# Kernel tuning notes

Measured on AMD Instinct MI355X. Metric: run time of the kernel, lower is better.

The kernel has to match this reference:

```python
import jax, jax.numpy as jnp
import numpy as np

N_NODES = 20000
N_EDGES = 160000
F_IN = 512
HIDDEN = 512
N_CLASSES = 40


def setup_inputs() -> dict:
    key = jax.random.key(0)
    k1, k2, k3, k4 = jax.random.split(key, 4)
    x = jax.random.normal(k1, (N_NODES, F_IN), dtype=jnp.float32)
    edge_index = jax.random.randint(k2, (2, N_EDGES), 0, N_NODES, dtype=jnp.int64)
    # Glorot-ish init scale for the linear weights
    W1 = jax.random.normal(k3, (F_IN, HIDDEN), dtype=jnp.float32) / np.sqrt(F_IN)
    b1 = jnp.zeros((HIDDEN,), dtype=jnp.float32)
    W2 = jax.random.normal(k4, (HIDDEN, N_CLASSES), dtype=jnp.float32) / np.sqrt(HIDDEN)
    b2 = jnp.zeros((N_CLASSES,), dtype=jnp.float32)
    return {"x": x, "edge_index": edge_index, "W1": W1, "b1": b1, "W2": W2, "b2": b2}


def _gcn_conv(x, W, b, src, dst, n_nodes):
    """PyG GCNConv: h = D^-1/2 (A+I) D^-1/2 (x W) + b, self-loops already in src/dst."""
    h = x @ W  # [N, out]
    deg = jax.ops.segment_sum(jnp.ones_like(dst, dtype=h.dtype), dst, num_segments=n_nodes)
    deg_inv_sqrt = jnp.where(deg > 0, jax.lax.rsqrt(jnp.maximum(deg, 1.0)), 0.0)
    norm = deg_inv_sqrt[src] * deg_inv_sqrt[dst]  # [E]
    msg = h[src] * norm[:, None]  # [E, out]
    return jax.ops.segment_sum(msg, dst, num_segments=n_nodes) + b


def reference(x, edge_index, W1, b1, W2, b2):
    n = x.shape[0]
    loop = jnp.arange(n, dtype=edge_index.dtype)
    src = jnp.concatenate([edge_index[0], loop])  # add self-loops
    dst = jnp.concatenate([edge_index[1], loop])
    h = _gcn_conv(x, W1, b1, src, dst, n)
    h = jax.nn.relu(h)
    # dropout(p=0.5) is identity in eval mode
    out = _gcn_conv(h, W2, b2, src, dst, n)
    return out
```

## Files before the change

kernel.cpp:

```cpp
#include <hip/hip_runtime.h>
#include <hip/hip_bf16.h>
#include <stdint.h>

#define N_NODES  20000
#define N_EDGES  160000
#define N_CLS    40
#define M_PAD    20096
#define CNT_PAD  20480
#define CAP      64

typedef __bf16 bf16;
typedef __attribute__((ext_vector_type(8))) __bf16 bf16x8;
typedef __attribute__((ext_vector_type(4))) float floatx4;

__device__ inline floatx4 zero4() { floatx4 z = {0.f, 0.f, 0.f, 0.f}; return z; }

typedef __attribute__((address_space(3))) uint32_t lds_u32;
typedef __attribute__((address_space(1))) const uint32_t glb_u32;
__device__ inline void ldst16(const bf16* g, bf16* l) {
    __builtin_amdgcn_global_load_lds((glb_u32*)g, (lds_u32*)l, 16, 0, 0);
}

struct Params {
    const float* x; const int* ei; const float* W1; const float* b1;
    const float* W2; const float* b2; float* out;
    bf16 *xb, *w1t, *w2p, *h1; float* h2;
    int *cnt, *colb;
};

#define S0_ZERO 20
#define S0_CONV 5024
#define S0_W1T  128
#define S0_W2P  96
#define S0_TOT  (S0_ZERO + S0_CONV + S0_W1T + S0_W2P)
#define NB_G1   640
#define NB_FILL 625

__global__ __launch_bounds__(256) void k_s0(Params p) {
    const int vb = blockIdx.x, tid = threadIdx.x;
    if (vb < S0_ZERO) {
        int4* dz = (int4*)(p.cnt) + vb * 256 + tid;
        *dz = make_int4(0, 0, 0, 0);
    } else if (vb < S0_ZERO + S0_CONV) {
        long e0 = ((long)(vb - S0_ZERO) * 256 + tid) * 8;
        int row = (int)(e0 >> 9);
        bf16x8 v;
        if (row < N_NODES) {
            const float4* ptr = (const float4*)(p.x + e0);
            float4 f0 = ptr[0], f1 = ptr[1];
            v[0] = (bf16)f0.x; v[1] = (bf16)f0.y; v[2] = (bf16)f0.z; v[3] = (bf16)f0.w;
            v[4] = (bf16)f1.x; v[5] = (bf16)f1.y; v[6] = (bf16)f1.z; v[7] = (bf16)f1.w;
        } else {
            for (int j = 0; j < 8; ++j) v[j] = (bf16)0.f;
        }
        *(bf16x8*)(p.xb + e0) = v;
    } else if (vb < S0_ZERO + S0_CONV + S0_W1T) {
        int t  = (vb - S0_ZERO - S0_CONV) * 256 + tid;
        int n  = t & 511;
        int k0 = (t >> 9) * 8;
        bf16x8 v;
        for (int j = 0; j < 8; ++j) v[j] = (bf16)p.W1[((k0 + j) << 9) + n];
        *(bf16x8*)(p.w1t + n * 512 + k0) = v;
    } else {
        int t = (vb - S0_ZERO - S0_CONV - S0_W1T) * 256 + tid;
        int j = t & 7; int e = t >> 3;
        int lane = e & 63; e >>= 6;
        int nb = e % 3; int kt = e / 3;
        int k = kt * 32 + (lane >> 4) * 8 + j;
        int n = nb * 16 + (lane & 15);
        float v = (n < N_CLS) ? p.W2[k * N_CLS + n] : 0.f;
        p.w2p[t] = (bf16)v;
    }
}

__global__ __launch_bounds__(256) void k_g1f(Params p) {
    if (blockIdx.x >= NB_G1) {
        int e = (blockIdx.x - NB_G1) * 256 + threadIdx.x;
        if (e < N_EDGES) {
            int d = p.ei[N_EDGES + e];
            int j = atomicAdd(&p.cnt[d], 1);
            if (j < CAP) p.colb[d * CAP + j] = p.ei[e];
        }
        return;
    }
    const int g  = blockIdx.x;
    const int mi = (g >> 5) * 8 + (g & 7);
    const int ni = (g >> 3) & 3;
    if (mi >= 157) return;
    __shared__ bf16 As[2][128 * 32];
    __shared__ bf16 Bs[2][128 * 32];
    const int tid  = threadIdx.x;
    const int lane = tid & 63;
    const int w    = tid >> 6;
    const int wm   = w >> 1, wn = w & 1;
    const int m0   = mi * 128;
    const int n0   = ni * 128;
    const int fr   = lane & 15, fq = lane >> 4;

    floatx4 acc[4][4];
    for (int mb = 0; mb < 4; ++mb)
        for (int nb = 0; nb < 4; ++nb) acc[mb][nb] = zero4();

    const int sr = lane >> 2;
    const int sk = (lane & 3) * 8;
    const bf16* Ag = p.xb  + (long)(m0 + w * 32 + sr) * 512 + sk;
    const bf16* Bg = p.w1t + (long)(n0 + w * 32 + sr) * 512 + sk;
    const int wof = w * 1024;

    ldst16(Ag,            As[0] + wof);
    ldst16(Ag + 16 * 512, As[0] + wof + 512);
    ldst16(Bg,            Bs[0] + wof);
    ldst16(Bg + 16 * 512, Bs[0] + wof + 512);

    for (int kt = 0; kt < 16; ++kt) {
        const int cur = kt & 1, nxt = cur ^ 1;
        __syncthreads();
        if (kt < 15) {
            const int k1 = (kt + 1) * 32;
            ldst16(Ag + k1,            As[nxt] + wof);
            ldst16(Ag + k1 + 16 * 512, As[nxt] + wof + 512);
            ldst16(Bg + k1,            Bs[nxt] + wof);
            ldst16(Bg + k1 + 16 * 512, Bs[nxt] + wof + 512);
        }
        bf16x8 af[4], bfv[4];
        for (int mb = 0; mb < 4; ++mb)
            af[mb]  = *(const bf16x8*)(As[cur] + (wm * 64 + mb * 16 + fr) * 32 + fq * 8);
        for (int nb = 0; nb < 4; ++nb)
            bfv[nb] = *(const bf16x8*)(Bs[cur] + (wn * 64 + nb * 16 + fr) * 32 + fq * 8);
        for (int mb = 0; mb < 4; ++mb)
            for (int nb = 0; nb < 4; ++nb)
                acc[mb][nb] = __builtin_amdgcn_mfma_f32_16x16x32_bf16(af[mb], bfv[nb], acc[mb][nb], 0, 0, 0);
    }
    for (int mb = 0; mb < 4; ++mb)
        for (int nb = 0; nb < 4; ++nb) {
            int row0 = m0 + wm * 64 + mb * 16 + fq * 4;
            int c    = n0 + wn * 64 + nb * 16 + fr;
            for (int r = 0; r < 4; ++r)
                p.h1[(long)(row0 + r) * 512 + c] = (bf16)acc[mb][nb][r];
        }
}

__global__ __launch_bounds__(256) void k_agg1g2(Params p) {
    __shared__ bf16 t[16 * 512];
    const int tid = threadIdx.x, l = tid & 63, w = tid >> 6;
    const int ib = blockIdx.x * 16;

    const float4* bp = (const float4*)(p.b1 + l * 8);
    float4 c0 = bp[0], c1 = bp[1];
    float bb[8] = {c0.x, c0.y, c0.z, c0.w, c1.x, c1.y, c1.z, c1.w};

    for (int q4 = 0; q4 < 4; ++q4) {
        const int r = w * 4 + q4;
        const int i = ib + r;
        bf16x8 o;
        if (i >= N_NODES) {
            for (int j = 0; j < 8; ++j) o[j] = (bf16)0.f;
        } else {
            const int ci = p.cnt[i];
            const float di = rsqrtf((float)(ci + 1));
            float acc[8];
            {
                bf16x8 v = *(const bf16x8*)(p.h1 + (long)i * 512 + l * 8);
                const float wi = di * di;
                for (int j = 0; j < 8; ++j) acc[j] = (float)v[j] * wi;
            }
            const int e1 = ci < CAP ? ci : CAP;
            const int* rowcol = p.colb + (long)i * CAP;
            int e = 0;
            for (; e + 8 <= e1; e += 8) {
                int4 sa = *(const int4*)(rowcol + e);
                int4 sb = *(const int4*)(rowcol + e + 4);
                float wgt[8];
                wgt[0] = rsqrtf((float)(p.cnt[sa.x] + 1)) * di;
                wgt[1] = rsqrtf((float)(p.cnt[sa.y] + 1)) * di;
                wgt[2] = rsqrtf((float)(p.cnt[sa.z] + 1)) * di;
                wgt[3] = rsqrtf((float)(p.cnt[sa.w] + 1)) * di;
                wgt[4] = rsqrtf((float)(p.cnt[sb.x] + 1)) * di;
                wgt[5] = rsqrtf((float)(p.cnt[sb.y] + 1)) * di;
                wgt[6] = rsqrtf((float)(p.cnt[sb.z] + 1)) * di;
                wgt[7] = rsqrtf((float)(p.cnt[sb.w] + 1)) * di;
                bf16x8 u[8];
                u[0] = *(const bf16x8*)(p.h1 + (long)sa.x * 512 + l * 8);
                u[1] = *(const bf16x8*)(p.h1 + (long)sa.y * 512 + l * 8);
                u[2] = *(const bf16x8*)(p.h1 + (long)sa.z * 512 + l * 8);
                u[3] = *(const bf16x8*)(p.h1 + (long)sa.w * 512 + l * 8);
                u[4] = *(const bf16x8*)(p.h1 + (long)sb.x * 512 + l * 8);
                u[5] = *(const bf16x8*)(p.h1 + (long)sb.y * 512 + l * 8);
                u[6] = *(const bf16x8*)(p.h1 + (long)sb.z * 512 + l * 8);
                u[7] = *(const bf16x8*)(p.h1 + (long)sb.w * 512 + l * 8);
                for (int q = 0; q < 8; ++q)
                    for (int j = 0; j < 8; ++j) acc[j] += (float)u[q][j] * wgt[q];
            }
            for (; e + 4 <= e1; e += 4) {
                int4 ss = *(const int4*)(rowcol + e);
                float w0 = rsqrtf((float)(p.cnt[ss.x] + 1)) * di;
                float w1 = rsqrtf((float)(p.cnt[ss.y] + 1)) * di;
                float w2 = rsqrtf((float)(p.cnt[ss.z] + 1)) * di;
                float w3 = rsqrtf((float)(p.cnt[ss.w] + 1)) * di;
                bf16x8 u0 = *(const bf16x8*)(p.h1 + (long)ss.x * 512 + l * 8);
                bf16x8 u1 = *(const bf16x8*)(p.h1 + (long)ss.y * 512 + l * 8);
                bf16x8 u2 = *(const bf16x8*)(p.h1 + (long)ss.z * 512 + l * 8);
                bf16x8 u3 = *(const bf16x8*)(p.h1 + (long)ss.w * 512 + l * 8);
                for (int j = 0; j < 8; ++j)
                    acc[j] += (float)u0[j] * w0 + (float)u1[j] * w1 + (float)u2[j] * w2 + (float)u3[j] * w3;
            }
            for (; e < e1; ++e) {
                int s = rowcol[e];
                float wt = rsqrtf((float)(p.cnt[s] + 1)) * di;
                bf16x8 u = *(const bf16x8*)(p.h1 + (long)s * 512 + l * 8);
                for (int j = 0; j < 8; ++j) acc[j] += (float)u[j] * wt;
            }
            for (int j = 0; j < 8; ++j) {
                float f = acc[j] + bb[j];
                f = f > 0.f ? f : 0.f;
                o[j] = (bf16)f;
            }
        }
        *(bf16x8*)((char*)t + r * 1024 + ((l * 16) ^ ((r & 7) << 4))) = o;
    }
    __syncthreads();
    if (w < 3) {
        const int fr = l & 15, fq = l >> 4;
        const int nb = w;
        floatx4 acc2 = zero4();
        for (int kt = 0; kt < 16; ++kt) {
            bf16x8 af = *(const bf16x8*)((const char*)t + fr * 1024 +
                                         ((kt * 64 + fq * 16) ^ ((fr & 7) << 4)));
            bf16x8 bfr = *(const bf16x8*)(p.w2p + ((kt * 3 + nb) * 64 + l) * 8);
            acc2 = __builtin_amdgcn_mfma_f32_16x16x32_bf16(af, bfr, acc2, 0, 0, 0);
        }
        for (int r2 = 0; r2 < 4; ++r2)
            p.h2[(long)(ib + fq * 4 + r2) * 48 + nb * 16 + fr] = acc2[r2];
    }
}

__global__ __launch_bounds__(256) void k_agg2(Params p) {
    const int i = blockIdx.x * 4 + (threadIdx.x >> 6);
    const int l = threadIdx.x & 63;
    if (i >= N_NODES || l >= N_CLS) return;
    const int ci = p.cnt[i];
    const float di = rsqrtf((float)(ci + 1));
    float acc = p.h2[(long)i * 48 + l] * di * di;
    const int e1 = ci < CAP ? ci : CAP;
    const int* rowcol = p.colb + (long)i * CAP;
    int e = 0;
    for (; e + 4 <= e1; e += 4) {
        int4 ss = *(const int4*)(rowcol + e);
        acc += p.h2[(long)ss.x * 48 + l] * (rsqrtf((float)(p.cnt[ss.x] + 1)) * di)
             + p.h2[(long)ss.y * 48 + l] * (rsqrtf((float)(p.cnt[ss.y] + 1)) * di)
             + p.h2[(long)ss.z * 48 + l] * (rsqrtf((float)(p.cnt[ss.z] + 1)) * di)
             + p.h2[(long)ss.w * 48 + l] * (rsqrtf((float)(p.cnt[ss.w] + 1)) * di);
    }
    for (; e < e1; ++e) {
        int s = rowcol[e];
        acc += p.h2[(long)s * 48 + l] * (rsqrtf((float)(p.cnt[s] + 1)) * di);
    }
    p.out[(long)i * N_CLS + l] = acc + p.b2[l];
}


extern "C" void kernel_launch(void* const* d_in, const int* in_sizes, int n_in,
                              void* d_out, int out_size, void* d_ws, size_t ws_size,
                              hipStream_t stream) {
    Params p;
    p.x  = (const float*)d_in[0];
    p.ei = (const int*)d_in[1];
    p.W1 = (const float*)d_in[2];
    p.b1 = (const float*)d_in[3];
    p.W2 = (const float*)d_in[4];
    p.b2 = (const float*)d_in[5];
    p.out = (float*)d_out;

    char* base = (char*)d_ws;
    size_t o = 0;
    auto alloc = [&](size_t bytes) { size_t r = o; o = (o + bytes + 255) & ~(size_t)255; return r; };
    p.xb   = (bf16*)(base + alloc((size_t)M_PAD * 512 * 2));
    p.w1t  = (bf16*)(base + alloc((size_t)512 * 512 * 2));
    p.w2p  = (bf16*)(base + alloc((size_t)24576 * 2));
    p.h1   = (bf16*)(base + alloc((size_t)M_PAD * 512 * 2));
    p.h2   = (float*)(base + alloc((size_t)M_PAD * 48 * 4));
    p.cnt  = (int*)(base + alloc((size_t)CNT_PAD * 4));
    p.colb = (int*)(base + alloc((size_t)N_NODES * CAP * 4));

    k_s0    <<<S0_TOT,           256, 0, stream>>>(p);
    k_g1f   <<<NB_G1 + NB_FILL,  256, 0, stream>>>(p);
    k_agg1g2<<<M_PAD / 16,       256, 0, stream>>>(p);
    k_agg2  <<<N_NODES / 4,      256, 0, stream>>>(p);
}
```

Baseline: 153.8 us.

## Fuse fp32-to-bf16 conversion of x into GEMM tile loading

Removes the separate pass that converts x to a bf16 copy. The first-layer GEMM now streams fp32 x tiles directly into LDS and converts them to bf16 while building MFMA fragments. XOR swizzles are added to both the A and B LDS layouts to reduce bank conflicts. This saves one full write and read of the bf16 copy of x, at the cost of twice the A-tile LDS footprint and traffic, extra conversion work in the inner loop, and the fp32 x being re-read by each of the four column-block tiles.

```diff
diff --git a/kernel.cpp b/kernel.cpp
--- a/kernel.cpp
+++ b/kernel.cpp
@@ -17,22 +17,21 @@
 
 typedef __attribute__((address_space(3))) uint32_t lds_u32;
 typedef __attribute__((address_space(1))) const uint32_t glb_u32;
-__device__ inline void ldst16(const bf16* g, bf16* l) {
+__device__ inline void ldst16(const void* g, void* l) {
     __builtin_amdgcn_global_load_lds((glb_u32*)g, (lds_u32*)l, 16, 0, 0);
 }
 
 struct Params {
     const float* x; const int* ei; const float* W1; const float* b1;
     const float* W2; const float* b2; float* out;
-    bf16 *xb, *w1t, *w2p, *h1; float* h2;
+    bf16 *w1t, *w2p, *h1; float* h2;
     int *cnt, *colb;
 };
 
 #define S0_ZERO 20
-#define S0_CONV 5024
 #define S0_W1T  128
 #define S0_W2P  96
-#define S0_TOT  (S0_ZERO + S0_CONV + S0_W1T + S0_W2P)
+#define S0_TOT  (S0_ZERO + S0_W1T + S0_W2P)
 #define NB_G1   640
 #define NB_FILL 625
 
@@ -41,28 +40,15 @@
     if (vb < S0_ZERO) {
         int4* dz = (int4*)(p.cnt) + vb * 256 + tid;
         *dz = make_int4(0, 0, 0, 0);
-    } else if (vb < S0_ZERO + S0_CONV) {
-        long e0 = ((long)(vb - S0_ZERO) * 256 + tid) * 8;
-        int row = (int)(e0 >> 9);
-        bf16x8 v;
-        if (row < N_NODES) {
-            const float4* ptr = (const float4*)(p.x + e0);
-            float4 f0 = ptr[0], f1 = ptr[1];
-            v[0] = (bf16)f0.x; v[1] = (bf16)f0.y; v[2] = (bf16)f0.z; v[3] = (bf16)f0.w;
-            v[4] = (bf16)f1.x; v[5] = (bf16)f1.y; v[6] = (bf16)f1.z; v[7] = (bf16)f1.w;
-        } else {
-            for (int j = 0; j < 8; ++j) v[j] = (bf16)0.f;
-        }
-        *(bf16x8*)(p.xb + e0) = v;
-    } else if (vb < S0_ZERO + S0_CONV + S0_W1T) {
-        int t  = (vb - S0_ZERO - S0_CONV) * 256 + tid;
+    } else if (vb < S0_ZERO + S0_W1T) {
+        int t  = (vb - S0_ZERO) * 256 + tid;
         int n  = t & 511;
         int k0 = (t >> 9) * 8;
         bf16x8 v;
         for (int j = 0; j < 8; ++j) v[j] = (bf16)p.W1[((k0 + j) << 9) + n];
         *(bf16x8*)(p.w1t + n * 512 + k0) = v;
     } else {
-        int t = (vb - S0_ZERO - S0_CONV - S0_W1T) * 256 + tid;
+        int t = (vb - S0_ZERO - S0_W1T) * 256 + tid;
         int j = t & 7; int e = t >> 3;
         int lane = e & 63; e >>= 6;
         int nb = e % 3; int kt = e / 3;
@@ -87,8 +73,8 @@
     const int mi = (g >> 5) * 8 + (g & 7);
     const int ni = (g >> 3) & 3;
     if (mi >= 157) return;
-    __shared__ bf16 As[2][128 * 32];
-    __shared__ bf16 Bs[2][128 * 32];
+    __shared__ float Asf[2][128 * 32];
+    __shared__ bf16  Bs[2][128 * 32];
     const int tid  = threadIdx.x;
     const int lane = tid & 63;
     const int w    = tid >> 6;
@@ -101,32 +87,52 @@
     for (int mb = 0; mb < 4; ++mb)
         for (int nb = 0; nb < 4; ++nb) acc[mb][nb] = zero4();
 
-    const int sr = lane >> 2;
-    const int sk = (lane & 3) * 8;
-    const bf16* Ag = p.xb  + (long)(m0 + w * 32 + sr) * 512 + sk;
-    const bf16* Bg = p.w1t + (long)(n0 + w * 32 + sr) * 512 + sk;
-    const int wof = w * 1024;
-
-    ldst16(Ag,            As[0] + wof);
-    ldst16(Ag + 16 * 512, As[0] + wof + 512);
-    ldst16(Bg,            Bs[0] + wof);
-    ldst16(Bg + 16 * 512, Bs[0] + wof + 512);
+    const int sr  = lane >> 2;
+    const int skB = (((lane & 3) ^ ((lane >> 3) & 3))) * 8;
+    const bf16* Bg = p.w1t + (long)(n0 + w * 32 + sr) * 512 + skB;
+
+    const int arl = lane >> 3;
+    const int ac  = (lane & 7) ^ arl;
+    const float* Agp[4];
+    for (int q = 0; q < 4; ++q) {
+        int gr = m0 + w * 32 + q * 8 + arl;
+        if (gr > N_NODES - 1) gr = N_NODES - 1;
+        Agp[q] = p.x + (long)gr * 512 + ac * 4;
+    }
+    const int wofA = w * 1024;
+    const int wofB = w * 1024;
+
+    for (int q = 0; q < 4; ++q)
+        ldst16(Agp[q], Asf[0] + wofA + q * 256);
+    ldst16(Bg,            Bs[0] + wofB);
+    ldst16(Bg + 16 * 512, Bs[0] + wofB + 512);
+
+    const int fqsB = (fq ^ ((fr >> 1) & 3)) * 8;
+    const int sA0  = (((fq << 1)    ) ^ (fr & 7)) * 4;
+    const int sA1  = (((fq << 1) | 1) ^ (fr & 7)) * 4;
 
     for (int kt = 0; kt < 16; ++kt) {
         const int cur = kt & 1, nxt = cur ^ 1;
         __syncthreads();
         if (kt < 15) {
             const int k1 = (kt + 1) * 32;
-            ldst16(Ag + k1,            As[nxt] + wof);
-            ldst16(Ag + k1 + 16 * 512, As[nxt] + wof + 512);
-            ldst16(Bg + k1,            Bs[nxt] + wof);
-            ldst16(Bg + k1 + 16 * 512, Bs[nxt] + wof + 512);
+            for (int q = 0; q < 4; ++q)
+                ldst16(Agp[q] + k1, Asf[nxt] + wofA + q * 256);
+            ldst16(Bg + k1,            Bs[nxt] + wofB);
+            ldst16(Bg + k1 + 16 * 512, Bs[nxt] + wofB + 512);
         }
         bf16x8 af[4], bfv[4];
-        for (int mb = 0; mb < 4; ++mb)
-            af[mb]  = *(const bf16x8*)(As[cur] + (wm * 64 + mb * 16 + fr) * 32 + fq * 8);
+        for (int mb = 0; mb < 4; ++mb) {
+            const float* rp = Asf[cur] + (wm * 64 + mb * 16 + fr) * 32;
+            float4 lo = *(const float4*)(rp + sA0);
+            float4 hi = *(const float4*)(rp + sA1);
+            bf16x8 v;
+            v[0] = (bf16)lo.x; v[1] = (bf16)lo.y; v[2] = (bf16)lo.z; v[3] = (bf16)lo.w;
+            v[4] = (bf16)hi.x; v[5] = (bf16)hi.y; v[6] = (bf16)hi.z; v[7] = (bf16)hi.w;
+            af[mb] = v;
+        }
         for (int nb = 0; nb < 4; ++nb)
-            bfv[nb] = *(const bf16x8*)(Bs[cur] + (wn * 64 + nb * 16 + fr) * 32 + fq * 8);
+            bfv[nb] = *(const bf16x8*)(Bs[cur] + (wn * 64 + nb * 16 + fr) * 32 + fqsB);
         for (int mb = 0; mb < 4; ++mb)
             for (int nb = 0; nb < 4; ++nb)
                 acc[mb][nb] = __builtin_amdgcn_mfma_f32_16x16x32_bf16(af[mb], bfv[nb], acc[mb][nb], 0, 0, 0);
@@ -274,7 +280,6 @@
     char* base = (char*)d_ws;
     size_t o = 0;
     auto alloc = [&](size_t bytes) { size_t r = o; o = (o + bytes + 255) & ~(size_t)255; return r; };
-    p.xb   = (bf16*)(base + alloc((size_t)M_PAD * 512 * 2));
     p.w1t  = (bf16*)(base + alloc((size_t)512 * 512 * 2));
     p.w2p  = (bf16*)(base + alloc((size_t)24576 * 2));
     p.h1   = (bf16*)(base + alloc((size_t)M_PAD * 512 * 2));
```

New measurement: 152.4 us. Within noise of the previous version (-1.0%).
